# Optimization experiments

Hardware: AMD Instinct MI355X
Metric: run time of the kernel (lower is better)

## Reference

```python
import jax, jax.numpy as jnp
import numpy as np

K_SEL = 8        # selection budget K
R_ITER = 1       # fixed-point refinement steps r
LAM = 0.5        # lam
MAX_PROXY = 16   # max_proxy_points
KNN_K = 1        # knn_k = max(1, r)


def knn_stats(x, k):
    # x: [B,N,D] -> [B,N,4] stats of k nearest-neighbor distances (self excluded)
    sq = jnp.sum(x * x, axis=-1)
    d2 = sq[:, :, None] + sq[:, None, :] - 2.0 * jnp.einsum('bnd,bmd->bnm', x, x)
    n = x.shape[1]
    d2 = d2 + jnp.eye(n, dtype=x.dtype) * 1e9  # mask self-distance
    neg_vals, _ = jax.lax.top_k(-d2, k)        # k smallest distances
    d = jnp.sqrt(jnp.maximum(-neg_vals, 0.0))  # [B,N,k]
    return jnp.stack([d.mean(-1), d.min(-1), d.max(-1), d.std(-1)], axis=-1)


def build_structural(x, selection_weights=None, knn_k=KNN_K):
    feats = jnp.concatenate([x, knn_stats(x, knn_k)], axis=-1)
    if selection_weights is not None:
        feats = jnp.concatenate([feats, selection_weights[..., None]], axis=-1)
    return feats


def feature_similarity(f):
    fn = f / (jnp.linalg.norm(f, axis=-1, keepdims=True) + 1e-8)
    return jnp.einsum('bnd,bmd->bnm', fn, fn)


def soft_selector(saliency, similarity, log_temp):
    # SoftSelectorProxy.forward
    temp = jnp.clip(jnp.exp(log_temp), 0.1, 10.0)
    y = jax.nn.sigmoid((saliency / (2.0 * LAM) - 0.5) / temp)

    def rescale(y):
        budget = jnp.clip(y.sum(axis=1, keepdims=True), 1e-6, None)
        return y * jnp.minimum(K_SEL / budget, 1.0)

    y = rescale(y)
    for _ in range(R_ITER):
        overlap = jnp.einsum('bnm,bm->bn', similarity, y)
        y = rescale(y / (1.0 + overlap))
    return y


def setup_inputs() -> dict:
    key = jax.random.key(0)
    ks = jax.random.split(key, 8)
    B, N, D, H = 8, 2048, 32, 64
    K_LIFT, D_MODEL = 16, 256
    ANCHOR = D + 4  # structural_feature_dim(input_dim, include_selection=False)
    s = 0.02
    return {
        'x': jax.random.normal(ks[0], (B, N, D), dtype=jnp.float32),
        'log_temp': jnp.zeros((), dtype=jnp.float32),  # init_temperature=1.0
        'W1': jax.random.normal(ks[1], (D, H), dtype=jnp.float32) * s,
        'b1': jnp.zeros((H,), dtype=jnp.float32),
        'W2': jax.random.normal(ks[2], (H, 1), dtype=jnp.float32) * s,
        'b2': jnp.zeros((1,), dtype=jnp.float32),
        'mu': jnp.zeros((ANCHOR,), dtype=jnp.float32),
        'sigma': jnp.ones((ANCHOR,), dtype=jnp.float32),
        'Wl': jax.random.normal(ks[3], (ANCHOR, K_LIFT), dtype=jnp.float32) * s,
        'bl': jnp.zeros((K_LIFT,), dtype=jnp.float32),
        'Wp': jax.random.normal(ks[4], (K_LIFT, D_MODEL), dtype=jnp.float32) * s,
        'bp': jnp.zeros((D_MODEL,), dtype=jnp.float32),
    }


def reference(x, log_temp, W1, b1, W2, b2, mu, sigma, Wl, bl, Wp, bp):
    # CausalEventModel: per-point MLP saliency head
    h = jax.nn.relu(jnp.einsum('bnd,dh->bnh', x, W1) + b1)
    saliency = (jnp.einsum('bnh,ho->bno', h, W2) + b2)[..., 0]  # [B,N]

    structural = build_structural(x, selection_weights=saliency)
    similarity = feature_similarity(structural)                  # [B,N,N]
    y_star = soft_selector(saliency, similarity, log_temp)       # [B,N]

    dense = build_structural(x, selection_weights=None)          # [B,N,anchor]
    lifted = jnp.tanh(jnp.einsum('bna,ak->bnk', (dense - mu) / sigma, Wl) + bl)

    N = lifted.shape[1]
    K_eff = min(N, MAX_PROXY)
    _, top_idx = jax.lax.top_k(y_star, K_eff)                    # [B,K_eff]
    cloud = jnp.take_along_axis(lifted, top_idx[..., None], axis=1)  # [B,K_eff,k]
    tokens = jnp.einsum('bkc,cd->bkd', cloud, Wp) + bp           # [B,K_eff,d_model]
    return tokens, y_star
```

## Files before the change

### kernel.cpp

```cpp
#include <hip/hip_runtime.h>
#include <math.h>

#define B 8
#define N 2048
#define DIM 32
#define HID 64
#define KLIFT 16
#define DMODEL 256
#define KPROXY 16
#define KSEL 8.0f

typedef float f32x4 __attribute__((ext_vector_type(4)));
typedef short bf16x8 __attribute__((ext_vector_type(8)));

__device__ inline unsigned short f2bf(float f) {
  unsigned u = __float_as_uint(f);
  unsigned r = (u + 0x7FFFu + ((u >> 16) & 1u)) >> 16;
  return (unsigned short)r;
}
__device__ inline float bf2f(unsigned short s) {
  return __uint_as_float(((unsigned)s) << 16);
}
__device__ inline float clip_temp(float lt) {
  return fminf(fmaxf(expf(lt), 0.1f), 10.f);
}

__global__ __launch_bounds__(256) void k_prep(
    const float* __restrict__ x, const float* __restrict__ W1,
    const float* __restrict__ b1, const float* __restrict__ W2,
    const float* __restrict__ b2, const float* __restrict__ logt,
    float* __restrict__ sal, float* __restrict__ sq,
    unsigned short* __restrict__ Xhi, unsigned short* __restrict__ Xlo,
    float* __restrict__ partials1) {
  __shared__ float sW1[DIM * HID];
  __shared__ float sW2[HID], sb1[HID];
  __shared__ float red[4];
  int t = threadIdx.x;
  int lane = t & 63, wid = t >> 6;
  {
    const float4* s4 = (const float4*)W1;
    float4* d4 = (float4*)sW1;
    for (int i = t; i < DIM * HID / 4; i += 256) d4[i] = s4[i];
    if (t < HID) { sW2[t] = W2[t]; sb1[t] = b1[t]; }
  }
  __syncthreads();
  int p = blockIdx.x * 256 + t;
  float xr[DIM];
  const float4* xp = (const float4*)(x + (size_t)p * DIM);
#pragma unroll
  for (int i = 0; i < DIM / 4; i++) {
    float4 v = xp[i];
    xr[4 * i + 0] = v.x; xr[4 * i + 1] = v.y; xr[4 * i + 2] = v.z; xr[4 * i + 3] = v.w;
  }
  float s = 0.f;
#pragma unroll
  for (int d = 0; d < DIM; d++) s = fmaf(xr[d], xr[d], s);
  sq[p] = s;
  float h[HID];
#pragma unroll
  for (int j = 0; j < HID; j++) h[j] = sb1[j];
  for (int d = 0; d < DIM; d++) {
    float xv = xr[d];
    const float4* wrow = (const float4*)(&sW1[d * HID]);
#pragma unroll
    for (int j4 = 0; j4 < HID / 4; j4++) {
      float4 w = wrow[j4];
      h[4 * j4 + 0] = fmaf(xv, w.x, h[4 * j4 + 0]);
      h[4 * j4 + 1] = fmaf(xv, w.y, h[4 * j4 + 1]);
      h[4 * j4 + 2] = fmaf(xv, w.z, h[4 * j4 + 2]);
      h[4 * j4 + 3] = fmaf(xv, w.w, h[4 * j4 + 3]);
    }
  }
  float acc = b2[0];
#pragma unroll
  for (int j = 0; j < HID; j++) acc = fmaf(fmaxf(h[j], 0.f), sW2[j], acc);
  sal[p] = acc;
  float temp = clip_temp(logt[0]);
  float y0 = 1.f / (1.f + expf(-((acc - 0.5f) / temp)));
  float part = y0;
#pragma unroll
  for (int off = 32; off >= 1; off >>= 1) part += __shfl_xor(part, off);
  if (lane == 0) red[wid] = part;
  __syncthreads();
  if (t == 0) partials1[blockIdx.x] = red[0] + red[1] + red[2] + red[3];
  int bb = p >> 11, n = p & (N - 1);
  int tile = n >> 4, c = n & 15;
  size_t tb = ((size_t)(bb * 128 + tile)) * 64;
#pragma unroll
  for (int g = 0; g < 4; g++) {
    bf16x8 hv, lv;
#pragma unroll
    for (int j = 0; j < 8; j++) {
      float v = xr[g * 8 + j];
      unsigned short hb = f2bf(v);
      hv[j] = (short)hb;
      lv[j] = (short)f2bf(v - bf2f(hb));
    }
    size_t off = (tb + (size_t)g * 16 + c) * 8;
    *(bf16x8*)(Xhi + off) = hv;
    *(bf16x8*)(Xlo + off) = lv;
  }
}

__global__ __launch_bounds__(256) void k_nnd(
    const unsigned short* __restrict__ Xhi, const unsigned short* __restrict__ Xlo,
    const float* __restrict__ sq, const float* __restrict__ sal,
    const float* __restrict__ x, const float* __restrict__ logt,
    const float* __restrict__ partials1,
    float* __restrict__ nnd2f, float* __restrict__ gpart) {
  int bid = blockIdx.x;
  int bb = bid >> 5, nch = bid & 31;
  int t = threadIdx.x, w = t >> 6, lane = t & 63;
  int c = lane & 15, g = lane >> 4;
  int ntile = nch * 4 + w;
  __shared__ unsigned short ldsH[32 * 512];
  __shared__ unsigned short ldsL[32 * 512];
  __shared__ float ssq[512];
  __shared__ float dvs[64], cs[64];
  __shared__ float gsh[8][32];
  bf16x8 ah = *(const bf16x8*)(Xhi + (((size_t)(bb * 128 + ntile)) * 64 + lane) * 8);
  bf16x8 al = *(const bf16x8*)(Xlo + (((size_t)(bb * 128 + ntile)) * 64 + lane) * 8);
  float mn[4] = {1e30f, 1e30f, 1e30f, 1e30f};
  for (int mc = 0; mc < 4; mc++) {
    __syncthreads();
    size_t base = ((size_t)(bb * 128 + mc * 32)) * 512;
    const float4* srcH = (const float4*)(Xhi + base);
    const float4* srcL = (const float4*)(Xlo + base);
    float4* dH = (float4*)ldsH;
    float4* dL = (float4*)ldsL;
    for (int i = t; i < 2048; i += 256) { dH[i] = srcH[i]; dL[i] = srcL[i]; }
    ssq[t] = sq[bb * N + mc * 512 + t];
    ssq[t + 256] = sq[bb * N + mc * 512 + t + 256];
    __syncthreads();
    for (int tt = 0; tt < 32; tt++) {
      bf16x8 bh = ((const bf16x8*)(ldsH + tt * 512))[lane];
      bf16x8 bl2 = ((const bf16x8*)(ldsL + tt * 512))[lane];
      f32x4 a0 = {0.f, 0.f, 0.f, 0.f};
      a0 = __builtin_amdgcn_mfma_f32_16x16x32_bf16(ah, bh, a0, 0, 0, 0);
      a0 = __builtin_amdgcn_mfma_f32_16x16x32_bf16(ah, bl2, a0, 0, 0, 0);
      a0 = __builtin_amdgcn_mfma_f32_16x16x32_bf16(al, bh, a0, 0, 0, 0);
      float sm = ssq[tt * 16 + c];
      int mtg = mc * 32 + tt;
      bool diag = (mtg == ntile);
#pragma unroll
      for (int r = 0; r < 4; r++) {
        float v = fmaf(-2.f, a0[r], sm);
        if (diag && c == 4 * g + r) v = 1e30f;
        mn[r] = fminf(mn[r], v);
      }
    }
  }
#pragma unroll
  for (int off = 1; off <= 8; off <<= 1) {
#pragma unroll
    for (int r = 0; r < 4; r++) mn[r] = fminf(mn[r], __shfl_xor(mn[r], off));
  }
  if (c == 0) {
#pragma unroll
    for (int r = 0; r < 4; r++) {
      int n0 = ntile * 16 + 4 * g + r;
      float d2 = fmaxf(sq[bb * N + n0] + mn[r], 0.f);
      nnd2f[bb * N + n0] = d2;
      dvs[w * 16 + 4 * g + r] = sqrtf(d2);
    }
  }
  __syncthreads();
  float temp = clip_temp(logt[0]);
  if (t < 64) {
    int n = nch * 64 + t;
    size_t basep = (size_t)bb * N + n;
    float b1v = 0.f;
    for (int j = 0; j < 8; j++) b1v += partials1[bb * 8 + j];
    float scale1 = fminf(KSEL / fmaxf(b1v, 1e-6f), 1.f);
    float sv = sal[basep];
    float y0 = 1.f / (1.f + expf(-((sv - 0.5f) / temp)));
    float y1 = y0 * scale1;
    float dv = dvs[t];
    float nrm = sqrtf(sq[basep] + 3.f * dv * dv + sv * sv) + 1e-8f;
    float cn = y1 / nrm;
    cs[t] = cn;
    float v32 = cn * dv, v33 = cn * sv;
#pragma unroll
    for (int off = 32; off >= 1; off >>= 1) {
      v32 += __shfl_xor(v32, off);
      v33 += __shfl_xor(v33, off);
    }
    if (t == 0) {
      gpart[(size_t)(bb * 32 + nch) * 36 + 32] = v32;
      gpart[(size_t)(bb * 32 + nch) * 36 + 33] = v33;
    }
  }
  __syncthreads();
  int d = t & 31, pg = t >> 5;
  float acc = 0.f;
#pragma unroll
  for (int i = 0; i < 8; i++)
    acc = fmaf(cs[pg * 8 + i], x[((size_t)bb * N + nch * 64 + pg * 8 + i) * DIM + d], acc);
  gsh[pg][d] = acc;
  __syncthreads();
  if (t < 32) {
    float s = 0.f;
#pragma unroll
    for (int pgi = 0; pgi < 8; pgi++) s += gsh[pgi][t];
    gpart[(size_t)(bb * 32 + nch) * 36 + t] = s;
  }
}

__global__ __launch_bounds__(256) void k_c(
    const float* __restrict__ x, const float* __restrict__ sal,
    const float* __restrict__ sq, const float* __restrict__ nnd2f,
    const float* __restrict__ logt, const float* __restrict__ partials1,
    const float* __restrict__ gpart, float* __restrict__ partials2,
    float* __restrict__ ystar) {
  int bid = blockIdx.x;
  int bb = bid >> 3, ch = bid & 7;
  int t = threadIdx.x, lane = t & 63, wid = t >> 6;
  __shared__ float gfin[34];
  __shared__ float s1sh;
  __shared__ float red[4];
  if (t < 34) {
    float s = 0.f;
    for (int j = 0; j < 32; j++) s += gpart[(size_t)(bb * 32 + j) * 36 + t];
    gfin[t] = s;
  }
  if (t == 40) {
    float s = 0.f;
    for (int j = 0; j < 8; j++) s += partials1[bb * 8 + j];
    s1sh = fminf(KSEL / fmaxf(s, 1e-6f), 1.f);
  }
  __syncthreads();
  float scale1 = s1sh;
  int n = ch * 256 + t;
  size_t base = (size_t)bb * N + n;
  float temp = clip_temp(logt[0]);
  float sv = sal[base];
  float y0 = 1.f / (1.f + expf(-((sv - 0.5f) / temp)));
  float y1 = y0 * scale1;
  float dv = sqrtf(nnd2f[base]);
  float nrm = sqrtf(sq[base] + 3.f * dv * dv + sv * sv) + 1e-8f;
  const float4* p4 = (const float4*)(x + base * DIM);
  float ov = 0.f;
#pragma unroll
  for (int cc = 0; cc < 8; cc++) {
    float4 v = p4[cc];
    ov = fmaf(v.x, gfin[4 * cc + 0], ov);
    ov = fmaf(v.y, gfin[4 * cc + 1], ov);
    ov = fmaf(v.z, gfin[4 * cc + 2], ov);
    ov = fmaf(v.w, gfin[4 * cc + 3], ov);
  }
  ov += 3.f * dv * gfin[32] + sv * gfin[33];
  ov /= nrm;
  float y2 = y1 / (1.f + ov);
  ystar[base] = y2;
  float part = y2;
#pragma unroll
  for (int off = 32; off >= 1; off >>= 1) part += __shfl_xor(part, off);
  if (lane == 0) red[wid] = part;
  __syncthreads();
  if (t == 0) partials2[bb * 8 + ch] = red[0] + red[1] + red[2] + red[3];
}

__global__ __launch_bounds__(512) void k_post(
    const float* __restrict__ x, const float* __restrict__ nnd2f,
    const float* __restrict__ partials2, const float* __restrict__ mu,
    const float* __restrict__ sigma, const float* __restrict__ Wl,
    const float* __restrict__ bl, const float* __restrict__ Wp,
    const float* __restrict__ bp, float* __restrict__ tok,
    float* __restrict__ ystar) {
  int b = blockIdx.x, t = threadIdx.x;
  int lane = t & 63, wid = t >> 6;
  __shared__ float yv[N];
  __shared__ float bsh;
  __shared__ float candv[128];
  __shared__ int candi[128];
  __shared__ int tix[KPROXY];
  __shared__ float sz[KPROXY][36];
  if (t == 0) {
    float s = 0.f;
    for (int j = 0; j < 8; j++) s += partials2[b * 8 + j];
    bsh = fminf(KSEL / fmaxf(s, 1e-6f), 1.f);
  }
  __syncthreads();
  float scale2 = bsh;
#pragma unroll
  for (int i = 0; i < 4; i++) {
    int n = t + 512 * i;
    float y = ystar[(size_t)b * N + n] * scale2;
    yv[n] = y;
    ystar[(size_t)b * N + n] = y;
  }
  __syncthreads();
  float lv0 = yv[wid * 256 + lane];        int li0 = wid * 256 + lane;
  float lv1 = yv[wid * 256 + 64 + lane];   int li1 = li0 + 64;
  float lv2 = yv[wid * 256 + 128 + lane];  int li2 = li0 + 128;
  float lv3 = yv[wid * 256 + 192 + lane];  int li3 = li0 + 192;
  for (int r = 0; r < KPROXY; r++) {
    float bv = lv0; int bi = li0;
    if (lv1 > bv) { bv = lv1; bi = li1; }
    if (lv2 > bv) { bv = lv2; bi = li2; }
    if (lv3 > bv) { bv = lv3; bi = li3; }
#pragma unroll
    for (int off = 1; off < 64; off <<= 1) {
      float ovv = __shfl_xor(bv, off);
      int oi = __shfl_xor(bi, off);
      if (ovv > bv || (ovv == bv && oi < bi)) { bv = ovv; bi = oi; }
    }
    if (lane == 0) { candv[wid * 16 + r] = bv; candi[wid * 16 + r] = bi; }
    if (li0 == bi) lv0 = -1e30f;
    if (li1 == bi) lv1 = -1e30f;
    if (li2 == bi) lv2 = -1e30f;
    if (li3 == bi) lv3 = -1e30f;
  }
  __syncthreads();
  if (wid == 0) {
    float cv0 = candv[lane], cv1 = candv[lane + 64];
    int ci0 = candi[lane], ci1 = candi[lane + 64];
    for (int r = 0; r < KPROXY; r++) {
      float bv = cv0; int bi = ci0;
      if (cv1 > bv || (cv1 == bv && ci1 < bi)) { bv = cv1; bi = ci1; }
#pragma unroll
      for (int off = 1; off < 64; off <<= 1) {
        float ovv = __shfl_xor(bv, off);
        int oi = __shfl_xor(bi, off);
        if (ovv > bv || (ovv == bv && oi < bi)) { bv = ovv; bi = oi; }
      }
      if (lane == 0) tix[r] = bi;
      if (ci0 == bi) cv0 = -1e30f;
      if (ci1 == bi) cv1 = -1e30f;
    }
  }
  __syncthreads();
  for (int it = 0; it < 2; it++) {
    int k = wid + 8 * it;
    int srow = tix[k];
    if (lane < 36) {
      float f;
      if (lane < 32) f = x[((size_t)b * N + srow) * DIM + lane];
      else if (lane < 35) f = sqrtf(nnd2f[b * N + srow]);
      else f = 0.f;
      sz[k][lane] = (f - mu[lane]) / sigma[lane];
    }
    __syncthreads();
    float lf = 0.f;
    if (lane < KLIFT) {
      float a = bl[lane];
#pragma unroll
      for (int d = 0; d < 36; d++) a = fmaf(sz[k][d], Wl[d * KLIFT + lane], a);
      lf = tanhf(a);
    }
    float o0 = bp[lane], o1 = bp[lane + 64], o2 = bp[lane + 128], o3 = bp[lane + 192];
#pragma unroll
    for (int j = 0; j < KLIFT; j++) {
      float lj = __shfl(lf, j);
      const float* wr = Wp + j * DMODEL + lane;
      o0 = fmaf(lj, wr[0], o0);
      o1 = fmaf(lj, wr[64], o1);
      o2 = fmaf(lj, wr[128], o2);
      o3 = fmaf(lj, wr[192], o3);
    }
    float* tp = tok + ((size_t)b * KPROXY + k) * DMODEL + lane;
    tp[0] = o0; tp[64] = o1; tp[128] = o2; tp[192] = o3;
  }
}

extern "C" void kernel_launch(void* const* d_in, const int* in_sizes, int n_in,
                              void* d_out, int out_size, void* d_ws, size_t ws_size,
                              hipStream_t stream) {
  const float* x  = (const float*)d_in[0];
  const float* lt = (const float*)d_in[1];
  const float* W1 = (const float*)d_in[2];
  const float* b1 = (const float*)d_in[3];
  const float* W2 = (const float*)d_in[4];
  const float* b2 = (const float*)d_in[5];
  const float* mu = (const float*)d_in[6];
  const float* sg = (const float*)d_in[7];
  const float* Wl = (const float*)d_in[8];
  const float* bl = (const float*)d_in[9];
  const float* Wp = (const float*)d_in[10];
  const float* bp = (const float*)d_in[11];

  float* tok = (float*)d_out;
  float* ystar = tok + B * KPROXY * DMODEL;

  char* ws = (char*)d_ws;
  float* sal          = (float*)(ws);
  float* sq           = (float*)(ws + 65536);
  float* nnd2f        = (float*)(ws + 131072);
  float* partials1    = (float*)(ws + 196608);
  float* gpart        = (float*)(ws + 197120);
  float* partials2    = (float*)(ws + 234496);
  unsigned short* Xhi = (unsigned short*)(ws + 262144);
  unsigned short* Xlo = (unsigned short*)(ws + 262144 + 1048576);

  k_prep<<<B * N / 256, 256, 0, stream>>>(x, W1, b1, W2, b2, lt, sal, sq, Xhi, Xlo, partials1);
  k_nnd<<<B * 32, 256, 0, stream>>>(Xhi, Xlo, sq, sal, x, lt, partials1, nnd2f, gpart);
  k_c<<<B * 8, 256, 0, stream>>>(x, sal, sq, nnd2f, lt, partials1, gpart, partials2, ystar);
  k_post<<<B, 512, 0, stream>>>(x, nnd2f, partials2, mu, sg, Wl, bl, Wp, bp, tok, ystar);
}
```

Measured before the change: 67.40 us.

## Split nearest-neighbor search over column chunks with atomicMin merge and separate reduction kernel

The kNN distance kernel now splits the 2048 candidate columns into 8 chunks per block and gives each wave two row tiles. This raises the grid from 256 to 1024 blocks and reuses each LDS-loaded B tile across two A tiles. Partial minima are merged with atomicMin on the float bit pattern, which works because the values are non-negative, and k_prep initializes the buffer. The similarity-weighted partial sums move into a new k_c1 kernel that stages x in LDS. This adds one kernel launch and atomic traffic in exchange for better CU occupancy on the dominant all-pairs pass.

```diff
diff --git a/kernel.cpp b/kernel.cpp
--- a/kernel.cpp
+++ b/kernel.cpp
@@ -31,7 +31,7 @@
     const float* __restrict__ b2, const float* __restrict__ logt,
     float* __restrict__ sal, float* __restrict__ sq,
     unsigned short* __restrict__ Xhi, unsigned short* __restrict__ Xlo,
-    float* __restrict__ partials1) {
+    float* __restrict__ partials1, unsigned* __restrict__ nnd2) {
   __shared__ float sW1[DIM * HID];
   __shared__ float sW2[HID], sb1[HID];
   __shared__ float red[4];
@@ -45,6 +45,7 @@
   }
   __syncthreads();
   int p = blockIdx.x * 256 + t;
+  nnd2[p] = 0x7F7F7F7Fu;
   float xr[DIM];
   const float4* xp = (const float4*)(x + (size_t)p * DIM);
 #pragma unroll
@@ -104,111 +105,142 @@
 
 __global__ __launch_bounds__(256) void k_nnd(
     const unsigned short* __restrict__ Xhi, const unsigned short* __restrict__ Xlo,
-    const float* __restrict__ sq, const float* __restrict__ sal,
-    const float* __restrict__ x, const float* __restrict__ logt,
-    const float* __restrict__ partials1,
-    float* __restrict__ nnd2f, float* __restrict__ gpart) {
+    const float* __restrict__ sq, unsigned* __restrict__ nnd2) {
   int bid = blockIdx.x;
-  int bb = bid >> 5, nch = bid & 31;
-  int t = threadIdx.x, w = t >> 6, lane = t & 63;
+  int bb = bid >> 7;
+  int nch = (bid >> 3) & 15;
+  int mo = bid & 7;
+  int t = threadIdx.x;
+  int w = t >> 6, lane = t & 63;
   int c = lane & 15, g = lane >> 4;
-  int ntile = nch * 4 + w;
-  __shared__ unsigned short ldsH[32 * 512];
-  __shared__ unsigned short ldsL[32 * 512];
-  __shared__ float ssq[512];
-  __shared__ float dvs[64], cs[64];
-  __shared__ float gsh[8][32];
-  bf16x8 ah = *(const bf16x8*)(Xhi + (((size_t)(bb * 128 + ntile)) * 64 + lane) * 8);
-  bf16x8 al = *(const bf16x8*)(Xlo + (((size_t)(bb * 128 + ntile)) * 64 + lane) * 8);
-  float mn[4] = {1e30f, 1e30f, 1e30f, 1e30f};
-  for (int mc = 0; mc < 4; mc++) {
-    __syncthreads();
-    size_t base = ((size_t)(bb * 128 + mc * 32)) * 512;
+  __shared__ unsigned short ldsH[16 * 512];
+  __shared__ unsigned short ldsL[16 * 512];
+  __shared__ float ssq[256];
+  {
+    size_t base = ((size_t)(bb * 128 + mo * 16)) * 512;
     const float4* srcH = (const float4*)(Xhi + base);
     const float4* srcL = (const float4*)(Xlo + base);
     float4* dH = (float4*)ldsH;
     float4* dL = (float4*)ldsL;
-    for (int i = t; i < 2048; i += 256) { dH[i] = srcH[i]; dL[i] = srcL[i]; }
-    ssq[t] = sq[bb * N + mc * 512 + t];
-    ssq[t + 256] = sq[bb * N + mc * 512 + t + 256];
-    __syncthreads();
-    for (int tt = 0; tt < 32; tt++) {
-      bf16x8 bh = ((const bf16x8*)(ldsH + tt * 512))[lane];
-      bf16x8 bl2 = ((const bf16x8*)(ldsL + tt * 512))[lane];
-      f32x4 a0 = {0.f, 0.f, 0.f, 0.f};
-      a0 = __builtin_amdgcn_mfma_f32_16x16x32_bf16(ah, bh, a0, 0, 0, 0);
-      a0 = __builtin_amdgcn_mfma_f32_16x16x32_bf16(ah, bl2, a0, 0, 0, 0);
-      a0 = __builtin_amdgcn_mfma_f32_16x16x32_bf16(al, bh, a0, 0, 0, 0);
-      float sm = ssq[tt * 16 + c];
-      int mtg = mc * 32 + tt;
-      bool diag = (mtg == ntile);
-#pragma unroll
-      for (int r = 0; r < 4; r++) {
-        float v = fmaf(-2.f, a0[r], sm);
-        if (diag && c == 4 * g + r) v = 1e30f;
-        mn[r] = fminf(mn[r], v);
-      }
+    for (int i = t; i < 1024; i += 256) { dH[i] = srcH[i]; dL[i] = srcL[i]; }
+    ssq[t] = sq[bb * N + mo * 256 + t];
+  }
+  int nt0 = nch * 8 + w * 2, nt1 = nt0 + 1;
+  bf16x8 ah0 = *(const bf16x8*)(Xhi + (((size_t)(bb * 128 + nt0)) * 64 + lane) * 8);
+  bf16x8 al0 = *(const bf16x8*)(Xlo + (((size_t)(bb * 128 + nt0)) * 64 + lane) * 8);
+  bf16x8 ah1 = *(const bf16x8*)(Xhi + (((size_t)(bb * 128 + nt1)) * 64 + lane) * 8);
+  bf16x8 al1 = *(const bf16x8*)(Xlo + (((size_t)(bb * 128 + nt1)) * 64 + lane) * 8);
+  __syncthreads();
+  float mn0[4] = {1e30f, 1e30f, 1e30f, 1e30f};
+  float mn1[4] = {1e30f, 1e30f, 1e30f, 1e30f};
+  for (int tt = 0; tt < 16; tt++) {
+    bf16x8 bh = ((const bf16x8*)(ldsH + tt * 512))[lane];
+    bf16x8 bl2 = ((const bf16x8*)(ldsL + tt * 512))[lane];
+    f32x4 a0 = {0.f, 0.f, 0.f, 0.f};
+    f32x4 a1 = {0.f, 0.f, 0.f, 0.f};
+    a0 = __builtin_amdgcn_mfma_f32_16x16x32_bf16(ah0, bh, a0, 0, 0, 0);
+    a1 = __builtin_amdgcn_mfma_f32_16x16x32_bf16(ah1, bh, a1, 0, 0, 0);
+    a0 = __builtin_amdgcn_mfma_f32_16x16x32_bf16(ah0, bl2, a0, 0, 0, 0);
+    a1 = __builtin_amdgcn_mfma_f32_16x16x32_bf16(ah1, bl2, a1, 0, 0, 0);
+    a0 = __builtin_amdgcn_mfma_f32_16x16x32_bf16(al0, bh, a0, 0, 0, 0);
+    a1 = __builtin_amdgcn_mfma_f32_16x16x32_bf16(al1, bh, a1, 0, 0, 0);
+    float sm = ssq[tt * 16 + c];
+    int mtg = mo * 16 + tt;
+    bool d0 = (mtg == nt0), d1 = (mtg == nt1);
+#pragma unroll
+    for (int r = 0; r < 4; r++) {
+      float v0 = fmaf(-2.f, a0[r], sm);
+      float v1 = fmaf(-2.f, a1[r], sm);
+      if (d0 && c == 4 * g + r) v0 = 1e30f;
+      if (d1 && c == 4 * g + r) v1 = 1e30f;
+      mn0[r] = fminf(mn0[r], v0);
+      mn1[r] = fminf(mn1[r], v1);
     }
   }
 #pragma unroll
   for (int off = 1; off <= 8; off <<= 1) {
 #pragma unroll
-    for (int r = 0; r < 4; r++) mn[r] = fminf(mn[r], __shfl_xor(mn[r], off));
+    for (int r = 0; r < 4; r++) {
+      mn0[r] = fminf(mn0[r], __shfl_xor(mn0[r], off));
+      mn1[r] = fminf(mn1[r], __shfl_xor(mn1[r], off));
+    }
   }
   if (c == 0) {
 #pragma unroll
     for (int r = 0; r < 4; r++) {
-      int n0 = ntile * 16 + 4 * g + r;
-      float d2 = fmaxf(sq[bb * N + n0] + mn[r], 0.f);
-      nnd2f[bb * N + n0] = d2;
-      dvs[w * 16 + 4 * g + r] = sqrtf(d2);
-    }
-  }
-  __syncthreads();
+      int n0 = nt0 * 16 + 4 * g + r;
+      float v = fmaxf(sq[bb * N + n0] + mn0[r], 0.f);
+      atomicMin(&nnd2[bb * N + n0], __float_as_uint(v));
+      int n1 = nt1 * 16 + 4 * g + r;
+      v = fmaxf(sq[bb * N + n1] + mn1[r], 0.f);
+      atomicMin(&nnd2[bb * N + n1], __float_as_uint(v));
+    }
+  }
+}
+
+__global__ __launch_bounds__(256) void k_c1(
+    const float* __restrict__ x, const float* __restrict__ sal,
+    const float* __restrict__ sq, const unsigned* __restrict__ nnd2,
+    const float* __restrict__ logt, const float* __restrict__ partials1,
+    float* __restrict__ gpart) {
+  int bid = blockIdx.x;
+  int bb = bid >> 3, ch = bid & 7;
+  int t = threadIdx.x, lane = t & 63, wid = t >> 6;
+  __shared__ float xs[256][33];
+  __shared__ float cs[256];
+  __shared__ float gsh[8][32];
+  __shared__ float red32[4], red33[4];
+  int n = ch * 256 + t;
+  size_t base = (size_t)bb * N + n;
   float temp = clip_temp(logt[0]);
-  if (t < 64) {
-    int n = nch * 64 + t;
-    size_t basep = (size_t)bb * N + n;
-    float b1v = 0.f;
-    for (int j = 0; j < 8; j++) b1v += partials1[bb * 8 + j];
-    float scale1 = fminf(KSEL / fmaxf(b1v, 1e-6f), 1.f);
-    float sv = sal[basep];
-    float y0 = 1.f / (1.f + expf(-((sv - 0.5f) / temp)));
-    float y1 = y0 * scale1;
-    float dv = dvs[t];
-    float nrm = sqrtf(sq[basep] + 3.f * dv * dv + sv * sv) + 1e-8f;
-    float cn = y1 / nrm;
-    cs[t] = cn;
-    float v32 = cn * dv, v33 = cn * sv;
-#pragma unroll
-    for (int off = 32; off >= 1; off >>= 1) {
-      v32 += __shfl_xor(v32, off);
-      v33 += __shfl_xor(v33, off);
-    }
-    if (t == 0) {
-      gpart[(size_t)(bb * 32 + nch) * 36 + 32] = v32;
-      gpart[(size_t)(bb * 32 + nch) * 36 + 33] = v33;
-    }
-  }
-  __syncthreads();
+  float b1v = 0.f;
+  for (int j = 0; j < 8; j++) b1v += partials1[bb * 8 + j];
+  float scale1 = fminf(KSEL / fmaxf(b1v, 1e-6f), 1.f);
+  float sv = sal[base];
+  float y0 = 1.f / (1.f + expf(-((sv - 0.5f) / temp)));
+  float y1 = y0 * scale1;
+  float dv = sqrtf(__uint_as_float(nnd2[base]));
+  float nrm = sqrtf(sq[base] + 3.f * dv * dv + sv * sv) + 1e-8f;
+  float cn = y1 / nrm;
+  cs[t] = cn;
+  {
+    const float4* xsrc = (const float4*)(x + ((size_t)bb * N + ch * 256) * DIM);
+    for (int j = t; j < 2048; j += 256) {
+      float4 v = xsrc[j];
+      int pt = j >> 3, c4 = (j & 7) * 4;
+      xs[pt][c4 + 0] = v.x; xs[pt][c4 + 1] = v.y;
+      xs[pt][c4 + 2] = v.z; xs[pt][c4 + 3] = v.w;
+    }
+  }
+  float v32 = cn * dv, v33 = cn * sv;
+#pragma unroll
+  for (int off = 32; off >= 1; off >>= 1) {
+    v32 += __shfl_xor(v32, off);
+    v33 += __shfl_xor(v33, off);
+  }
+  if (lane == 0) { red32[wid] = v32; red33[wid] = v33; }
+  __syncthreads();
+  if (t == 0) {
+    gpart[(size_t)(bb * 8 + ch) * 36 + 32] = red32[0] + red32[1] + red32[2] + red32[3];
+    gpart[(size_t)(bb * 8 + ch) * 36 + 33] = red33[0] + red33[1] + red33[2] + red33[3];
+  }
   int d = t & 31, pg = t >> 5;
   float acc = 0.f;
 #pragma unroll
-  for (int i = 0; i < 8; i++)
-    acc = fmaf(cs[pg * 8 + i], x[((size_t)bb * N + nch * 64 + pg * 8 + i) * DIM + d], acc);
+  for (int i = 0; i < 32; i++) acc = fmaf(cs[pg * 32 + i], xs[pg * 32 + i][d], acc);
   gsh[pg][d] = acc;
   __syncthreads();
   if (t < 32) {
     float s = 0.f;
 #pragma unroll
     for (int pgi = 0; pgi < 8; pgi++) s += gsh[pgi][t];
-    gpart[(size_t)(bb * 32 + nch) * 36 + t] = s;
+    gpart[(size_t)(bb * 8 + ch) * 36 + t] = s;
   }
 }
 
 __global__ __launch_bounds__(256) void k_c(
     const float* __restrict__ x, const float* __restrict__ sal,
-    const float* __restrict__ sq, const float* __restrict__ nnd2f,
+    const float* __restrict__ sq, const unsigned* __restrict__ nnd2,
     const float* __restrict__ logt, const float* __restrict__ partials1,
     const float* __restrict__ gpart, float* __restrict__ partials2,
     float* __restrict__ ystar) {
@@ -220,7 +252,7 @@
   __shared__ float red[4];
   if (t < 34) {
     float s = 0.f;
-    for (int j = 0; j < 32; j++) s += gpart[(size_t)(bb * 32 + j) * 36 + t];
+    for (int j = 0; j < 8; j++) s += gpart[(size_t)(bb * 8 + j) * 36 + t];
     gfin[t] = s;
   }
   if (t == 40) {
@@ -236,7 +268,7 @@
   float sv = sal[base];
   float y0 = 1.f / (1.f + expf(-((sv - 0.5f) / temp)));
   float y1 = y0 * scale1;
-  float dv = sqrtf(nnd2f[base]);
+  float dv = sqrtf(__uint_as_float(nnd2[base]));
   float nrm = sqrtf(sq[base] + 3.f * dv * dv + sv * sv) + 1e-8f;
   const float4* p4 = (const float4*)(x + base * DIM);
   float ov = 0.f;
@@ -261,7 +293,7 @@
 }
 
 __global__ __launch_bounds__(512) void k_post(
-    const float* __restrict__ x, const float* __restrict__ nnd2f,
+    const float* __restrict__ x, const unsigned* __restrict__ nnd2,
     const float* __restrict__ partials2, const float* __restrict__ mu,
     const float* __restrict__ sigma, const float* __restrict__ Wl,
     const float* __restrict__ bl, const float* __restrict__ Wp,
@@ -336,7 +368,7 @@
     if (lane < 36) {
       float f;
       if (lane < 32) f = x[((size_t)b * N + srow) * DIM + lane];
-      else if (lane < 35) f = sqrtf(nnd2f[b * N + srow]);
+      else if (lane < 35) f = sqrtf(__uint_as_float(nnd2[b * N + srow]));
       else f = 0.f;
       sz[k][lane] = (f - mu[lane]) / sigma[lane];
     }
@@ -385,15 +417,16 @@
   char* ws = (char*)d_ws;
   float* sal          = (float*)(ws);
   float* sq           = (float*)(ws + 65536);
-  float* nnd2f        = (float*)(ws + 131072);
+  unsigned* nnd2      = (unsigned*)(ws + 131072);
   float* partials1    = (float*)(ws + 196608);
   float* gpart        = (float*)(ws + 197120);
-  float* partials2    = (float*)(ws + 234496);
+  float* partials2    = (float*)(ws + 231424);
   unsigned short* Xhi = (unsigned short*)(ws + 262144);
   unsigned short* Xlo = (unsigned short*)(ws + 262144 + 1048576);
 
-  k_prep<<<B * N / 256, 256, 0, stream>>>(x, W1, b1, W2, b2, lt, sal, sq, Xhi, Xlo, partials1);
-  k_nnd<<<B * 32, 256, 0, stream>>>(Xhi, Xlo, sq, sal, x, lt, partials1, nnd2f, gpart);
-  k_c<<<B * 8, 256, 0, stream>>>(x, sal, sq, nnd2f, lt, partials1, gpart, partials2, ystar);
-  k_post<<<B, 512, 0, stream>>>(x, nnd2f, partials2, mu, sg, Wl, bl, Wp, bp, tok, ystar);
-}
+  k_prep<<<B * N / 256, 256, 0, stream>>>(x, W1, b1, W2, b2, lt, sal, sq, Xhi, Xlo, partials1, nnd2);
+  k_nnd<<<B * 16 * 8, 256, 0, stream>>>(Xhi, Xlo, sq, nnd2);
+  k_c1<<<B * 8, 256, 0, stream>>>(x, sal, sq, nnd2, lt, partials1, gpart);
+  k_c<<<B * 8, 256, 0, stream>>>(x, sal, sq, nnd2, lt, partials1, gpart, partials2, ystar);
+  k_post<<<B, 512, 0, stream>>>(x, nnd2, partials2, mu, sg, Wl, bl, Wp, bp, tok, ystar);
+}
```

Result: faster. 60.18 us (-10.7%).
